# Kernel tuning notes

Measured on AMD Instinct MI355X. Metric: run time of the kernel, lower is better.

The kernel has to match this reference:

```python
import jax, jax.numpy as jnp
import numpy as np

N_NODES, SEQ_LEN, IN_CH, HID, OUT_CH, N_EDGES = 10000, 12, 16, 64, 1, 160000


def setup_inputs() -> dict:
    key = jax.random.key(0)
    ks = jax.random.split(key, 16)
    s = 1.0 / np.sqrt(HID)
    u = lambda k, shape: jax.random.uniform(k, shape, jnp.float32, -s, s)
    return {
        "x_seq": jax.random.normal(ks[0], (1, SEQ_LEN, N_NODES, IN_CH), jnp.float32),
        "edge_index": jax.random.randint(ks[1], (2, N_EDGES), 0, N_NODES, jnp.int32),
        "gcn_w": jax.random.normal(ks[2], (IN_CH, HID), jnp.float32) / np.sqrt(IN_CH),
        "gcn_b": jnp.zeros((HID,), jnp.float32),
        "w_ih0": u(ks[3], (3 * HID, HID)),
        "w_hh0": u(ks[4], (3 * HID, HID)),
        "b_ih0": u(ks[5], (3 * HID,)),
        "b_hh0": u(ks[6], (3 * HID,)),
        "w_ih1": u(ks[7], (3 * HID, HID)),
        "w_hh1": u(ks[8], (3 * HID, HID)),
        "b_ih1": u(ks[9], (3 * HID,)),
        "b_hh1": u(ks[10], (3 * HID,)),
        "attn_w": u(ks[11], (HID, 1)),
        "attn_b": u(ks[12], (1,)),
        "fc_w": u(ks[13], (HID, OUT_CH)),
        "fc_b": u(ks[14], (OUT_CH,)),
    }


def _gcn_all_t(x_ntf, edge_index, w, b):
    # x_ntf: (N, T, F). Symmetric-normalized GCNConv with self loops (PyG default),
    # applied to every timestep at once (edge structure is static).
    n = x_ntf.shape[0]
    loop = jnp.arange(n, dtype=edge_index.dtype)
    src = jnp.concatenate([edge_index[0], loop])
    dst = jnp.concatenate([edge_index[1], loop])
    deg = jax.ops.segment_sum(jnp.ones_like(src, dtype=x_ntf.dtype), dst, num_segments=n)
    dis = jax.lax.rsqrt(deg)  # deg >= 1 thanks to self loops
    norm = dis[src] * dis[dst]  # (E+N,)
    msg = x_ntf[src] * norm[:, None, None]  # (E+N, T, F)
    agg = jax.ops.segment_sum(msg, dst, num_segments=n)  # (N, T, F)
    return agg @ w + b  # (N, T, H)


def _gru_layer(x, w_ih, w_hh, b_ih, b_hh):
    # x: (B, T, Hin) batch_first; PyTorch GRU cell equations, h0 = 0.
    bsz, _, _ = x.shape
    h_dim = w_hh.shape[1]
    xi = x @ w_ih.T + b_ih  # (B, T, 3H), precomputed input projections

    def step(h, xt):
        gh = h @ w_hh.T + b_hh
        ir, iz, in_ = jnp.split(xt, 3, axis=-1)
        hr, hz, hn = jnp.split(gh, 3, axis=-1)
        r = jax.nn.sigmoid(ir + hr)
        z = jax.nn.sigmoid(iz + hz)
        n = jnp.tanh(in_ + r * hn)
        h_new = (1.0 - z) * n + z * h
        return h_new, h_new

    h0 = jnp.zeros((bsz, h_dim), x.dtype)
    _, hs = jax.lax.scan(step, h0, jnp.swapaxes(xi, 0, 1))  # (T, B, H)
    return jnp.swapaxes(hs, 0, 1)


def reference(x_seq, edge_index, gcn_w, gcn_b, w_ih0, w_hh0, b_ih0, b_hh0,
              w_ih1, w_hh1, b_ih1, b_hh1, attn_w, attn_b, fc_w, fc_b):
    batch, seq_len, num_nodes, _ = x_seq.shape  # batch == 1 (see notes)
    # (B, T, N, F) -> (N, T, F)
    x_ntf = jnp.swapaxes(x_seq[0], 0, 1)
    gcn_out = jax.nn.relu(_gcn_all_t(x_ntf, edge_index, gcn_w, gcn_b))  # (N, T, H)
    # gru_input: (B*N, T, H); dropout between GRU layers disabled (inference)
    h1 = _gru_layer(gcn_out, w_ih0, w_hh0, b_ih0, b_hh0)
    gru_out = _gru_layer(h1, w_ih1, w_hh1, b_ih1, b_hh1)  # (N, T, H)
    attn_scores = jax.nn.softmax(gru_out @ attn_w + attn_b, axis=1)  # (N, T, 1)
    context = jnp.sum(attn_scores * gru_out, axis=1)  # (N, H)
    residual = (context @ fc_w + fc_b).reshape(batch, num_nodes, -1)
    last_known = x_seq[:, -1, :, 0][..., None]  # (B, N, 1)
    return last_known + residual
```

## Files before the change

### kernel.cpp

```cpp
#include <hip/hip_runtime.h>
#include <hip/hip_bf16.h>
#include <hip/hip_fp16.h>

#define N_NODES 10000
#define SEQ_T 12
#define IN_CH 16
#define HID 64
#define N_EDGES 160000
#define CAP 96
#define PB 0xAAAAAAAAu

typedef __attribute__((ext_vector_type(8))) short short8;
typedef __attribute__((ext_vector_type(4))) float floatx4;

__device__ __forceinline__ float frcp(float x){ return __builtin_amdgcn_rcpf(x); }
__device__ __forceinline__ float sigmf(float x){ return frcp(1.0f + __expf(-x)); }
__device__ __forceinline__ float tanh_fast(float x){ return 1.0f - 2.0f * frcp(1.0f + __expf(2.0f * x)); }
__device__ __forceinline__ unsigned short f2bf(float f){
  union { float f; unsigned int u; } c; c.f = f;
  unsigned int u = c.u;
  return (unsigned short)((u + 0x7FFFu + ((u >> 16) & 1u)) >> 16);
}
__device__ __forceinline__ unsigned short f2h(float f){
  _Float16 h = (_Float16)f; unsigned short u; __builtin_memcpy(&u, &h, 2); return u;
}
__device__ __forceinline__ unsigned int cvt_pk_bf16(float a, float b){
  unsigned int r;
  asm("v_cvt_pk_bf16_f32 %0, %1, %2" : "=v"(r) : "v"(a), "v"(b));
  return r;
}


__global__ void k_fill(const int* __restrict__ ei, unsigned int* __restrict__ cnt,
                       int* __restrict__ csr,
                       const float* __restrict__ wih0, const float* __restrict__ whh0,
                       const float* __restrict__ wih1, const float* __restrict__ whh1,
                       unsigned short* __restrict__ wF,
                       const float* __restrict__ x, unsigned short* __restrict__ xT){
  int i = blockIdx.x * 256 + threadIdx.x;
  if (i < 49152){
    const float* srcs[4] = {wih0, whh0, wih1, whh1};
    int p = i / 12288, ii = i - p * 12288;
    int e = ii & 7, l = (ii >> 3) & 63, jk = ii >> 9;
    int kt = jk / 12, jt = jk - kt * 12;
    int j = (l & 15) + 16 * jt;
    int k = ((l >> 4) * 8) + e + 32 * kt;
    wF[i] = f2bf(srcs[p][j * 64 + k]);
  }
  {
    int n = i >> 4, ch = i & 15;
    const float* xp = x + (size_t)n * IN_CH + ch;
    unsigned short tmp[SEQ_T];
    #pragma unroll
    for (int t = 0; t < SEQ_T; ++t) tmp[t] = f2h(xp[(size_t)t * N_NODES * IN_CH]);
    unsigned short* dp = xT + (size_t)n * 192 + ch * 12;
    *(ushort4*)(dp)     = make_ushort4(tmp[0], tmp[1], tmp[2],  tmp[3]);
    *(ushort4*)(dp + 4) = make_ushort4(tmp[4], tmp[5], tmp[6],  tmp[7]);
    *(ushort4*)(dp + 8) = make_ushort4(tmp[8], tmp[9], tmp[10], tmp[11]);
  }
  int s = ei[i], d = ei[N_EDGES + i];
  unsigned int pos = atomicAdd(&cnt[d], 1u) - PB;
  if (pos < CAP) csr[d * CAP + pos] = s;
}

__global__ __launch_bounds__(256, 3) void k_fused(
    const float* __restrict__ x, const unsigned short* __restrict__ xT,
    const unsigned int* __restrict__ cnt, const int* __restrict__ csr,
    const float* __restrict__ gcn_w, const float* __restrict__ gcn_b,
    const unsigned short* __restrict__ wF,
    const float* __restrict__ bih0, const float* __restrict__ bhh0,
    const float* __restrict__ bih1, const float* __restrict__ bhh1,
    const float* __restrict__ attn_w, const float* __restrict__ fc_w,
    const float* __restrict__ fc_b, float* __restrict__ out){
  __shared__ union {
    struct {
      float sm[SEQ_T][16][17];
      float smw[IN_CH * HID];
      float smb[HID];
      int2  eLDS[16][16];
    } A;
    struct {
      unsigned short HL[SEQ_T][16][72];
      float scdc[SEQ_T][2][16];
    } B;
  } U;
  __shared__ union {
    unsigned short gout[SEQ_T][1024];
    unsigned short h1[2][16][72];
  } V;

  const int tid = threadIdx.x;
  const int blk = blockIdx.x;

  {
    for (int i = tid; i < IN_CH * HID; i += 256) U.A.smw[i] = gcn_w[i];
    if (tid < HID) U.A.smb[tid] = gcn_b[tid];
    const int g = tid >> 4, ch = tid & 15;
    const int dst = blk * 16 + g;
    int deg = (int)(cnt[dst] - PB);
    if (deg > CAP) deg = CAP;
    float selfdis = rsqrtf((float)deg + 1.0f);
    __half2 ah[6];
    {
      const __half2* xs = (const __half2*)(const void*)(xT + (size_t)dst * 192 + ch * 12);
      __half2 sd2 = __float2half2_rn(selfdis);
      #pragma unroll
      for (int k = 0; k < 6; ++k) ah[k] = __hmul2(sd2, xs[k]);
    }
    for (int base = 0; base < deg; base += 16){
      int ep = base + ch;
      int2 ev = make_int2(0, 0);
      if (ep < deg){
        int s = csr[dst * CAP + ep];
        ev = make_int2(s, __float_as_int(rsqrtf((float)(cnt[s] - PB) + 1.0f)));
      }
      U.A.eLDS[g][ch] = ev;
      int c2 = deg - base; if (c2 > 16) c2 = 16;
      #pragma unroll 4
      for (int j = 0; j < c2; ++j){
        int2 e2 = U.A.eLDS[g][j];
        __half2 wh = __float2half2_rn(__int_as_float(e2.y));
        const __half2* xp = (const __half2*)(const void*)(xT + (size_t)e2.x * 192 + ch * 12);
        #pragma unroll
        for (int k = 0; k < 6; ++k) ah[k] = __hfma2(wh, xp[k], ah[k]);
      }
    }
    #pragma unroll
    for (int t = 0; t < SEQ_T; ++t){
      float f = (t & 1) ? __high2float(ah[t >> 1]) : __low2float(ah[t >> 1]);
      U.A.sm[t][g][ch] = selfdis * f;
    }
    __syncthreads();
    const int hq = tid & 15;
    float wreg[16][4];
    #pragma unroll
    for (int f = 0; f < 16; ++f)
      #pragma unroll
      for (int j = 0; j < 4; ++j) wreg[f][j] = U.A.smw[f * HID + hq * 4 + j];
    float b0 = U.A.smb[hq * 4],     b1 = U.A.smb[hq * 4 + 1],
          b2 = U.A.smb[hq * 4 + 2], b3 = U.A.smb[hq * 4 + 3];
    const int lb = (hq >> 3) * 512 + (g + 16 * ((hq >> 1) & 3)) * 8 + (hq & 1) * 4;
    #pragma unroll
    for (int t = 0; t < SEQ_T; ++t){
      float o0 = b0, o1 = b1, o2 = b2, o3 = b3;
      #pragma unroll
      for (int f = 0; f < 16; ++f){
        float v = U.A.sm[t][g][f];
        o0 = fmaf(v, wreg[f][0], o0);
        o1 = fmaf(v, wreg[f][1], o1);
        o2 = fmaf(v, wreg[f][2], o2);
        o3 = fmaf(v, wreg[f][3], o3);
      }
      unsigned int plo = cvt_pk_bf16(fmaxf(o0, 0.0f), fmaxf(o1, 0.0f));
      unsigned int phi = cvt_pk_bf16(fmaxf(o2, 0.0f), fmaxf(o3, 0.0f));
      *(uint2*)(void*)(&V.gout[t][lb]) = make_uint2(plo, phi);
    }
    __syncthreads();
  }

  const int w = tid >> 6;
  const int l = tid & 63;
  const int c = l & 15;
  const int q = l >> 4;
  const int hbase = 16 * w + 4 * q;

  {
    floatx4 brz4, bzz4, bin4, bhn4;
    #pragma unroll
    for (int r = 0; r < 4; ++r){
      brz4[r] = bih0[hbase + r] + bhh0[hbase + r];
      bzz4[r] = bih0[64 + hbase + r] + bhh0[64 + hbase + r];
      bin4[r] = bih0[128 + hbase + r];
      bhn4[r] = bhh0[128 + hbase + r];
    }
    short8 bw[2][3][2];
    #pragma unroll
    for (int g2 = 0; g2 < 2; ++g2)
      #pragma unroll
      for (int s = 0; s < 3; ++s)
        #pragma unroll
        for (int kt = 0; kt < 2; ++kt){
          int jt = w + 4 * s;
          size_t idx = ((((size_t)g2 * 2 + kt) * 12 + jt) * 64 + l) * 8;
          bw[g2][s][kt] = *(const short8*)(wF + idx);
        }
    float hp[4] = {0.f, 0.f, 0.f, 0.f};
    for (int t = 0; t < SEQ_T; ++t){
      short8 xa0 = *(const short8*)&V.gout[t][l * 8];
      short8 xa1 = *(const short8*)&V.gout[t][512 + l * 8];
      floatx4 aR = brz4, aZ = bzz4, aNx = bin4, aNh = bhn4;
      if (t > 0){
        short8 ha0 = *(const short8*)&U.B.HL[t - 1][c][8 * q];
        short8 ha1 = *(const short8*)&U.B.HL[t - 1][c][8 * q + 32];
        aR  = __builtin_amdgcn_mfma_f32_16x16x32_bf16(bw[1][0][0], ha0, aR, 0, 0, 0);
        aR  = __builtin_amdgcn_mfma_f32_16x16x32_bf16(bw[1][0][1], ha1, aR, 0, 0, 0);
        aZ  = __builtin_amdgcn_mfma_f32_16x16x32_bf16(bw[1][1][0], ha0, aZ, 0, 0, 0);
        aZ  = __builtin_amdgcn_mfma_f32_16x16x32_bf16(bw[1][1][1], ha1, aZ, 0, 0, 0);
        aNh = __builtin_amdgcn_mfma_f32_16x16x32_bf16(bw[1][2][0], ha0, aNh, 0, 0, 0);
        aNh = __builtin_amdgcn_mfma_f32_16x16x32_bf16(bw[1][2][1], ha1, aNh, 0, 0, 0);
      }
      aR  = __builtin_amdgcn_mfma_f32_16x16x32_bf16(bw[0][0][0], xa0, aR, 0, 0, 0);
      aR  = __builtin_amdgcn_mfma_f32_16x16x32_bf16(bw[0][0][1], xa1, aR, 0, 0, 0);
      aZ  = __builtin_amdgcn_mfma_f32_16x16x32_bf16(bw[0][1][0], xa0, aZ, 0, 0, 0);
      aZ  = __builtin_amdgcn_mfma_f32_16x16x32_bf16(bw[0][1][1], xa1, aZ, 0, 0, 0);
      aNx = __builtin_amdgcn_mfma_f32_16x16x32_bf16(bw[0][2][0], xa0, aNx, 0, 0, 0);
      aNx = __builtin_amdgcn_mfma_f32_16x16x32_bf16(bw[0][2][1], xa1, aNx, 0, 0, 0);
      float h4[4];
      #pragma unroll
      for (int r = 0; r < 4; ++r){
        float rr = sigmf(aR[r]);
        float zz = sigmf(aZ[r]);
        float nn = tanh_fast(aNx[r] + rr * aNh[r]);
        h4[r] = nn + zz * (hp[r] - nn);
        hp[r] = h4[r];
      }
      *(uint2*)(void*)(&U.B.HL[t][c][hbase]) =
          make_uint2(cvt_pk_bf16(h4[0], h4[1]), cvt_pk_bf16(h4[2], h4[3]));
      __syncthreads();
    }
  }

  short8 bwA[2];
  #pragma unroll
  for (int kt = 0; kt < 2; ++kt){
    short8 v;
    #pragma unroll
    for (int e = 0; e < 8; ++e){
      int k = q * 8 + e + 32 * kt;
      float f = (c == 0) ? attn_w[k] : (c == 1) ? fc_w[k] : 0.0f;
      v[e] = (short)f2bf(f);
    }
    bwA[kt] = v;
  }

  {
    floatx4 brz4, bzz4, bin4, bhn4;
    #pragma unroll
    for (int r = 0; r < 4; ++r){
      brz4[r] = bih1[hbase + r] + bhh1[hbase + r];
      bzz4[r] = bih1[64 + hbase + r] + bhh1[64 + hbase + r];
      bin4[r] = bih1[128 + hbase + r];
      bhn4[r] = bhh1[128 + hbase + r];
    }
    short8 bw[2][3][2];
    #pragma unroll
    for (int g2 = 0; g2 < 2; ++g2)
      #pragma unroll
      for (int s = 0; s < 3; ++s)
        #pragma unroll
        for (int kt = 0; kt < 2; ++kt){
          int jt = w + 4 * s;
          size_t idx = ((((size_t)(2 + g2) * 2 + kt) * 12 + jt) * 64 + l) * 8;
          bw[g2][s][kt] = *(const short8*)(wF + idx);
        }
    float hp[4] = {0.f, 0.f, 0.f, 0.f};
    for (int t = 0; t < SEQ_T; ++t){
      int pr = t & 1;
      short8 xa0 = *(const short8*)&U.B.HL[t][c][8 * q];
      short8 xa1 = *(const short8*)&U.B.HL[t][c][8 * q + 32];
      floatx4 aR = brz4, aZ = bzz4, aNx = bin4, aNh = bhn4;
      if (t > 0){
        short8 ha0 = *(const short8*)&V.h1[pr][c][8 * q];
        short8 ha1 = *(const short8*)&V.h1[pr][c][8 * q + 32];
        aR  = __builtin_amdgcn_mfma_f32_16x16x32_bf16(bw[1][0][0], ha0, aR, 0, 0, 0);
        aR  = __builtin_amdgcn_mfma_f32_16x16x32_bf16(bw[1][0][1], ha1, aR, 0, 0, 0);
        aZ  = __builtin_amdgcn_mfma_f32_16x16x32_bf16(bw[1][1][0], ha0, aZ, 0, 0, 0);
        aZ  = __builtin_amdgcn_mfma_f32_16x16x32_bf16(bw[1][1][1], ha1, aZ, 0, 0, 0);
        aNh = __builtin_amdgcn_mfma_f32_16x16x32_bf16(bw[1][2][0], ha0, aNh, 0, 0, 0);
        aNh = __builtin_amdgcn_mfma_f32_16x16x32_bf16(bw[1][2][1], ha1, aNh, 0, 0, 0);
        if (w == 0){
          floatx4 aA = (floatx4){0.f, 0.f, 0.f, 0.f};
          aA = __builtin_amdgcn_mfma_f32_16x16x32_bf16(bwA[0], ha0, aA, 0, 0, 0);
          aA = __builtin_amdgcn_mfma_f32_16x16x32_bf16(bwA[1], ha1, aA, 0, 0, 0);
          if (q == 0){
            U.B.scdc[t - 1][0][c] = aA[0];
            U.B.scdc[t - 1][1][c] = aA[1];
          }
        }
      }
      aR  = __builtin_amdgcn_mfma_f32_16x16x32_bf16(bw[0][0][0], xa0, aR, 0, 0, 0);
      aR  = __builtin_amdgcn_mfma_f32_16x16x32_bf16(bw[0][0][1], xa1, aR, 0, 0, 0);
      aZ  = __builtin_amdgcn_mfma_f32_16x16x32_bf16(bw[0][1][0], xa0, aZ, 0, 0, 0);
      aZ  = __builtin_amdgcn_mfma_f32_16x16x32_bf16(bw[0][1][1], xa1, aZ, 0, 0, 0);
      aNx = __builtin_amdgcn_mfma_f32_16x16x32_bf16(bw[0][2][0], xa0, aNx, 0, 0, 0);
      aNx = __builtin_amdgcn_mfma_f32_16x16x32_bf16(bw[0][2][1], xa1, aNx, 0, 0, 0);
      float h4[4];
      #pragma unroll
      for (int r = 0; r < 4; ++r){
        float rr = sigmf(aR[r]);
        float zz = sigmf(aZ[r]);
        float nn = tanh_fast(aNx[r] + rr * aNh[r]);
        h4[r] = nn + zz * (hp[r] - nn);
        hp[r] = h4[r];
      }
      *(uint2*)(void*)(&V.h1[1 - pr][c][hbase]) =
          make_uint2(cvt_pk_bf16(h4[0], h4[1]), cvt_pk_bf16(h4[2], h4[3]));
      __syncthreads();
    }
  }

  if (w == 0){
    short8 hL0 = *(const short8*)&V.h1[0][c][8 * q];
    short8 hL1 = *(const short8*)&V.h1[0][c][8 * q + 32];
    floatx4 aA = (floatx4){0.f, 0.f, 0.f, 0.f};
    aA = __builtin_amdgcn_mfma_f32_16x16x32_bf16(bwA[0], hL0, aA, 0, 0, 0);
    aA = __builtin_amdgcn_mfma_f32_16x16x32_bf16(bwA[1], hL1, aA, 0, 0, 0);
    if (q == 0){
      U.B.scdc[SEQ_T - 1][0][c] = aA[0];
      U.B.scdc[SEQ_T - 1][1][c] = aA[1];
    }
    int gn = blk * 16 + l;
    if (l < 16){
      float sc[SEQ_T], dc[SEQ_T];
      #pragma unroll
      for (int t = 0; t < SEQ_T; ++t){ sc[t] = U.B.scdc[t][0][l]; dc[t] = U.B.scdc[t][1][l]; }
      float m = sc[0];
      #pragma unroll
      for (int t = 1; t < SEQ_T; ++t) m = fmaxf(m, sc[t]);
      float den = 0.0f, num = 0.0f;
      #pragma unroll
      for (int t = 0; t < SEQ_T; ++t){
        float p = __expf(sc[t] - m);
        den += p;
        num = fmaf(p, dc[t], num);
      }
      float y = fc_b[0] + num * frcp(den);
      float last = x[((size_t)(SEQ_T - 1) * N_NODES + gn) * IN_CH];
      out[gn] = last + y;
    }
  }
}

extern "C" void kernel_launch(void* const* d_in, const int* in_sizes, int n_in,
                              void* d_out, int out_size, void* d_ws, size_t ws_size,
                              hipStream_t stream){
  const float* x = (const float*)d_in[0];
  const int* ei  = (const int*)d_in[1];
  char* ws = (char*)d_ws;
  unsigned int*   cnt = (unsigned int*)(ws);
  int*            csr = (int*)(ws + 40960);
  unsigned short* wF  = (unsigned short*)(ws + 3880960);
  unsigned short* xT  = (unsigned short*)(ws + 3979264);

  k_fill<<<625, 256, 0, stream>>>(ei, cnt, csr,
      (const float*)d_in[4], (const float*)d_in[5],
      (const float*)d_in[8], (const float*)d_in[9], wF,
      x, xT);
  k_fused<<<625, 256, 0, stream>>>(
      x, xT, cnt, csr,
      (const float*)d_in[2], (const float*)d_in[3], wF,
      (const float*)d_in[6],  (const float*)d_in[7],
      (const float*)d_in[10], (const float*)d_in[11],
      (const float*)d_in[12], (const float*)d_in[14], (const float*)d_in[15],
      (float*)d_out);
}
```

Measured before the change: 138.0 us.

## Interleave the two GRU layers in one software-pipelined time loop

The two sequential GRU layer loops are merged into one loop of SEQ_T+1 iterations: layer 1 computes step t while layer 0 computes step t+1, with one barrier per iteration. This roughly halves the number of block-wide barriers and gives the scheduler two independent MFMA and transcendental chains to overlap, aimed at cutting latency on the serial recurrence. Layer-0 outputs now go through a 2-deep ring buffer instead of a full 12-step buffer, and gout and h1 become separate shared arrays instead of a union. Both layers' weight fragments and biases are held in registers at once, which raises VGPR pressure under the 3-blocks-per-CU launch bound and risks spills. A small change in the fill kernel swaps a local pointer array for a ternary select.

Result: slower. 147.0 us (+6.5%).

```diff
diff --git a/kernel.cpp b/kernel.cpp
--- a/kernel.cpp
+++ b/kernel.cpp
@@ -39,13 +39,13 @@
                        const float* __restrict__ x, unsigned short* __restrict__ xT){
   int i = blockIdx.x * 256 + threadIdx.x;
   if (i < 49152){
-    const float* srcs[4] = {wih0, whh0, wih1, whh1};
     int p = i / 12288, ii = i - p * 12288;
+    const float* sp = (p & 2) ? ((p & 1) ? whh1 : wih1) : ((p & 1) ? whh0 : wih0);
     int e = ii & 7, l = (ii >> 3) & 63, jk = ii >> 9;
     int kt = jk / 12, jt = jk - kt * 12;
     int j = (l & 15) + 16 * jt;
     int k = ((l >> 4) * 8) + e + 32 * kt;
-    wF[i] = f2bf(srcs[p][j * 64 + k]);
+    wF[i] = f2bf(sp[j * 64 + k]);
   }
   {
     int n = i >> 4, ch = i & 15;
@@ -80,14 +80,12 @@
       int2  eLDS[16][16];
     } A;
     struct {
-      unsigned short HL[SEQ_T][16][72];
+      unsigned short HL[2][16][72];
       float scdc[SEQ_T][2][16];
     } B;
   } U;
-  __shared__ union {
-    unsigned short gout[SEQ_T][1024];
-    unsigned short h1[2][16][72];
-  } V;
+  __shared__ unsigned short gout[SEQ_T][1024];
+  __shared__ unsigned short h1[2][16][72];
 
   const int tid = threadIdx.x;
   const int blk = blockIdx.x;
@@ -153,7 +151,7 @@
       }
       unsigned int plo = cvt_pk_bf16(fmaxf(o0, 0.0f), fmaxf(o1, 0.0f));
       unsigned int phi = cvt_pk_bf16(fmaxf(o2, 0.0f), fmaxf(o3, 0.0f));
-      *(uint2*)(void*)(&V.gout[t][lb]) = make_uint2(plo, phi);
+      *(uint2*)(void*)(&gout[t][lb]) = make_uint2(plo, phi);
     }
     __syncthreads();
   }
@@ -164,144 +162,126 @@
   const int q = l >> 4;
   const int hbase = 16 * w + 4 * q;
 
-  {
-    floatx4 brz4, bzz4, bin4, bhn4;
-    #pragma unroll
-    for (int r = 0; r < 4; ++r){
-      brz4[r] = bih0[hbase + r] + bhh0[hbase + r];
-      bzz4[r] = bih0[64 + hbase + r] + bhh0[64 + hbase + r];
-      bin4[r] = bih0[128 + hbase + r];
-      bhn4[r] = bhh0[128 + hbase + r];
-    }
-    short8 bw[2][3][2];
-    #pragma unroll
-    for (int g2 = 0; g2 < 2; ++g2)
-      #pragma unroll
-      for (int s = 0; s < 3; ++s)
-        #pragma unroll
-        for (int kt = 0; kt < 2; ++kt){
-          int jt = w + 4 * s;
-          size_t idx = ((((size_t)g2 * 2 + kt) * 12 + jt) * 64 + l) * 8;
-          bw[g2][s][kt] = *(const short8*)(wF + idx);
-        }
-    float hp[4] = {0.f, 0.f, 0.f, 0.f};
-    for (int t = 0; t < SEQ_T; ++t){
-      short8 xa0 = *(const short8*)&V.gout[t][l * 8];
-      short8 xa1 = *(const short8*)&V.gout[t][512 + l * 8];
-      floatx4 aR = brz4, aZ = bzz4, aNx = bin4, aNh = bhn4;
-      if (t > 0){
-        short8 ha0 = *(const short8*)&U.B.HL[t - 1][c][8 * q];
-        short8 ha1 = *(const short8*)&U.B.HL[t - 1][c][8 * q + 32];
-        aR  = __builtin_amdgcn_mfma_f32_16x16x32_bf16(bw[1][0][0], ha0, aR, 0, 0, 0);
-        aR  = __builtin_amdgcn_mfma_f32_16x16x32_bf16(bw[1][0][1], ha1, aR, 0, 0, 0);
-        aZ  = __builtin_amdgcn_mfma_f32_16x16x32_bf16(bw[1][1][0], ha0, aZ, 0, 0, 0);
-        aZ  = __builtin_amdgcn_mfma_f32_16x16x32_bf16(bw[1][1][1], ha1, aZ, 0, 0, 0);
-        aNh = __builtin_amdgcn_mfma_f32_16x16x32_bf16(bw[1][2][0], ha0, aNh, 0, 0, 0);
-        aNh = __builtin_amdgcn_mfma_f32_16x16x32_bf16(bw[1][2][1], ha1, aNh, 0, 0, 0);
-      }
-      aR  = __builtin_amdgcn_mfma_f32_16x16x32_bf16(bw[0][0][0], xa0, aR, 0, 0, 0);
-      aR  = __builtin_amdgcn_mfma_f32_16x16x32_bf16(bw[0][0][1], xa1, aR, 0, 0, 0);
-      aZ  = __builtin_amdgcn_mfma_f32_16x16x32_bf16(bw[0][1][0], xa0, aZ, 0, 0, 0);
-      aZ  = __builtin_amdgcn_mfma_f32_16x16x32_bf16(bw[0][1][1], xa1, aZ, 0, 0, 0);
-      aNx = __builtin_amdgcn_mfma_f32_16x16x32_bf16(bw[0][2][0], xa0, aNx, 0, 0, 0);
-      aNx = __builtin_amdgcn_mfma_f32_16x16x32_bf16(bw[0][2][1], xa1, aNx, 0, 0, 0);
+  floatx4 brz0, bzz0, bin0, bhn0, brz1, bzz1, bin1, bhn1;
+  #pragma unroll
+  for (int r = 0; r < 4; ++r){
+    brz0[r] = bih0[hbase + r] + bhh0[hbase + r];
+    bzz0[r] = bih0[64 + hbase + r] + bhh0[64 + hbase + r];
+    bin0[r] = bih0[128 + hbase + r];
+    bhn0[r] = bhh0[128 + hbase + r];
+    brz1[r] = bih1[hbase + r] + bhh1[hbase + r];
+    bzz1[r] = bih1[64 + hbase + r] + bhh1[64 + hbase + r];
+    bin1[r] = bih1[128 + hbase + r];
+    bhn1[r] = bhh1[128 + hbase + r];
+  }
+  short8 bw0[2][3][2], bw1[2][3][2];
+  #pragma unroll
+  for (int g2 = 0; g2 < 2; ++g2)
+    #pragma unroll
+    for (int s = 0; s < 3; ++s)
+      #pragma unroll
+      for (int kt = 0; kt < 2; ++kt){
+        int jt = w + 4 * s;
+        bw0[g2][s][kt] = *(const short8*)(wF + ((((size_t)g2 * 2 + kt) * 12 + jt) * 64 + l) * 8);
+        bw1[g2][s][kt] = *(const short8*)(wF + ((((size_t)(2 + g2) * 2 + kt) * 12 + jt) * 64 + l) * 8);
+      }
+  short8 bwA[2];
+  #pragma unroll
+  for (int kt = 0; kt < 2; ++kt){
+    short8 v;
+    #pragma unroll
+    for (int e = 0; e < 8; ++e){
+      int k = q * 8 + e + 32 * kt;
+      float f = (c == 0) ? attn_w[k] : (c == 1) ? fc_w[k] : 0.0f;
+      v[e] = (short)f2bf(f);
+    }
+    bwA[kt] = v;
+  }
+
+  float hp0[4] = {0.f, 0.f, 0.f, 0.f};
+  float hp1[4] = {0.f, 0.f, 0.f, 0.f};
+  for (int i = 0; i <= SEQ_T; ++i){
+    if (i < SEQ_T){
+      short8 xa0 = *(const short8*)&gout[i][l * 8];
+      short8 xa1 = *(const short8*)&gout[i][512 + l * 8];
+      floatx4 aR = brz0, aZ = bzz0, aNx = bin0, aNh = bhn0;
+      if (i > 0){
+        short8 ha0 = *(const short8*)&U.B.HL[(i - 1) & 1][c][8 * q];
+        short8 ha1 = *(const short8*)&U.B.HL[(i - 1) & 1][c][8 * q + 32];
+        aR  = __builtin_amdgcn_mfma_f32_16x16x32_bf16(bw0[1][0][0], ha0, aR, 0, 0, 0);
+        aR  = __builtin_amdgcn_mfma_f32_16x16x32_bf16(bw0[1][0][1], ha1, aR, 0, 0, 0);
+        aZ  = __builtin_amdgcn_mfma_f32_16x16x32_bf16(bw0[1][1][0], ha0, aZ, 0, 0, 0);
+        aZ  = __builtin_amdgcn_mfma_f32_16x16x32_bf16(bw0[1][1][1], ha1, aZ, 0, 0, 0);
+        aNh = __builtin_amdgcn_mfma_f32_16x16x32_bf16(bw0[1][2][0], ha0, aNh, 0, 0, 0);
+        aNh = __builtin_amdgcn_mfma_f32_16x16x32_bf16(bw0[1][2][1], ha1, aNh, 0, 0, 0);
+      }
+      aR  = __builtin_amdgcn_mfma_f32_16x16x32_bf16(bw0[0][0][0], xa0, aR, 0, 0, 0);
+      aR  = __builtin_amdgcn_mfma_f32_16x16x32_bf16(bw0[0][0][1], xa1, aR, 0, 0, 0);
+      aZ  = __builtin_amdgcn_mfma_f32_16x16x32_bf16(bw0[0][1][0], xa0, aZ, 0, 0, 0);
+      aZ  = __builtin_amdgcn_mfma_f32_16x16x32_bf16(bw0[0][1][1], xa1, aZ, 0, 0, 0);
+      aNx = __builtin_amdgcn_mfma_f32_16x16x32_bf16(bw0[0][2][0], xa0, aNx, 0, 0, 0);
+      aNx = __builtin_amdgcn_mfma_f32_16x16x32_bf16(bw0[0][2][1], xa1, aNx, 0, 0, 0);
       float h4[4];
       #pragma unroll
       for (int r = 0; r < 4; ++r){
         float rr = sigmf(aR[r]);
         float zz = sigmf(aZ[r]);
         float nn = tanh_fast(aNx[r] + rr * aNh[r]);
-        h4[r] = nn + zz * (hp[r] - nn);
-        hp[r] = h4[r];
-      }
-      *(uint2*)(void*)(&U.B.HL[t][c][hbase]) =
+        h4[r] = nn + zz * (hp0[r] - nn);
+        hp0[r] = h4[r];
+      }
+      *(uint2*)(void*)(&U.B.HL[i & 1][c][hbase]) =
           make_uint2(cvt_pk_bf16(h4[0], h4[1]), cvt_pk_bf16(h4[2], h4[3]));
-      __syncthreads();
-    }
-  }
-
-  short8 bwA[2];
-  #pragma unroll
-  for (int kt = 0; kt < 2; ++kt){
-    short8 v;
-    #pragma unroll
-    for (int e = 0; e < 8; ++e){
-      int k = q * 8 + e + 32 * kt;
-      float f = (c == 0) ? attn_w[k] : (c == 1) ? fc_w[k] : 0.0f;
-      v[e] = (short)f2bf(f);
-    }
-    bwA[kt] = v;
-  }
-
-  {
-    floatx4 brz4, bzz4, bin4, bhn4;
-    #pragma unroll
-    for (int r = 0; r < 4; ++r){
-      brz4[r] = bih1[hbase + r] + bhh1[hbase + r];
-      bzz4[r] = bih1[64 + hbase + r] + bhh1[64 + hbase + r];
-      bin4[r] = bih1[128 + hbase + r];
-      bhn4[r] = bhh1[128 + hbase + r];
-    }
-    short8 bw[2][3][2];
-    #pragma unroll
-    for (int g2 = 0; g2 < 2; ++g2)
-      #pragma unroll
-      for (int s = 0; s < 3; ++s)
-        #pragma unroll
-        for (int kt = 0; kt < 2; ++kt){
-          int jt = w + 4 * s;
-          size_t idx = ((((size_t)(2 + g2) * 2 + kt) * 12 + jt) * 64 + l) * 8;
-          bw[g2][s][kt] = *(const short8*)(wF + idx);
-        }
-    float hp[4] = {0.f, 0.f, 0.f, 0.f};
-    for (int t = 0; t < SEQ_T; ++t){
+    }
+    if (i >= 1){
+      int t = i - 1;
       int pr = t & 1;
-      short8 xa0 = *(const short8*)&U.B.HL[t][c][8 * q];
-      short8 xa1 = *(const short8*)&U.B.HL[t][c][8 * q + 32];
-      floatx4 aR = brz4, aZ = bzz4, aNx = bin4, aNh = bhn4;
+      short8 xb0 = *(const short8*)&U.B.HL[pr][c][8 * q];
+      short8 xb1 = *(const short8*)&U.B.HL[pr][c][8 * q + 32];
+      floatx4 aR = brz1, aZ = bzz1, aNx = bin1, aNh = bhn1;
       if (t > 0){
-        short8 ha0 = *(const short8*)&V.h1[pr][c][8 * q];
-        short8 ha1 = *(const short8*)&V.h1[pr][c][8 * q + 32];
-        aR  = __builtin_amdgcn_mfma_f32_16x16x32_bf16(bw[1][0][0], ha0, aR, 0, 0, 0);
-        aR  = __builtin_amdgcn_mfma_f32_16x16x32_bf16(bw[1][0][1], ha1, aR, 0, 0, 0);
-        aZ  = __builtin_amdgcn_mfma_f32_16x16x32_bf16(bw[1][1][0], ha0, aZ, 0, 0, 0);
-        aZ  = __builtin_amdgcn_mfma_f32_16x16x32_bf16(bw[1][1][1], ha1, aZ, 0, 0, 0);
-        aNh = __builtin_amdgcn_mfma_f32_16x16x32_bf16(bw[1][2][0], ha0, aNh, 0, 0, 0);
-        aNh = __builtin_amdgcn_mfma_f32_16x16x32_bf16(bw[1][2][1], ha1, aNh, 0, 0, 0);
+        short8 hb0 = *(const short8*)&h1[pr][c][8 * q];
+        short8 hb1 = *(const short8*)&h1[pr][c][8 * q + 32];
+        aR  = __builtin_amdgcn_mfma_f32_16x16x32_bf16(bw1[1][0][0], hb0, aR, 0, 0, 0);
+        aR  = __builtin_amdgcn_mfma_f32_16x16x32_bf16(bw1[1][0][1], hb1, aR, 0, 0, 0);
+        aZ  = __builtin_amdgcn_mfma_f32_16x16x32_bf16(bw1[1][1][0], hb0, aZ, 0, 0, 0);
+        aZ  = __builtin_amdgcn_mfma_f32_16x16x32_bf16(bw1[1][1][1], hb1, aZ, 0, 0, 0);
+        aNh = __builtin_amdgcn_mfma_f32_16x16x32_bf16(bw1[1][2][0], hb0, aNh, 0, 0, 0);
+        aNh = __builtin_amdgcn_mfma_f32_16x16x32_bf16(bw1[1][2][1], hb1, aNh, 0, 0, 0);
         if (w == 0){
           floatx4 aA = (floatx4){0.f, 0.f, 0.f, 0.f};
-          aA = __builtin_amdgcn_mfma_f32_16x16x32_bf16(bwA[0], ha0, aA, 0, 0, 0);
-          aA = __builtin_amdgcn_mfma_f32_16x16x32_bf16(bwA[1], ha1, aA, 0, 0, 0);
+          aA = __builtin_amdgcn_mfma_f32_16x16x32_bf16(bwA[0], hb0, aA, 0, 0, 0);
+          aA = __builtin_amdgcn_mfma_f32_16x16x32_bf16(bwA[1], hb1, aA, 0, 0, 0);
           if (q == 0){
             U.B.scdc[t - 1][0][c] = aA[0];
             U.B.scdc[t - 1][1][c] = aA[1];
           }
         }
       }
-      aR  = __builtin_amdgcn_mfma_f32_16x16x32_bf16(bw[0][0][0], xa0, aR, 0, 0, 0);
-      aR  = __builtin_amdgcn_mfma_f32_16x16x32_bf16(bw[0][0][1], xa1, aR, 0, 0, 0);
-      aZ  = __builtin_amdgcn_mfma_f32_16x16x32_bf16(bw[0][1][0], xa0, aZ, 0, 0, 0);
-      aZ  = __builtin_amdgcn_mfma_f32_16x16x32_bf16(bw[0][1][1], xa1, aZ, 0, 0, 0);
-      aNx = __builtin_amdgcn_mfma_f32_16x16x32_bf16(bw[0][2][0], xa0, aNx, 0, 0, 0);
-      aNx = __builtin_amdgcn_mfma_f32_16x16x32_bf16(bw[0][2][1], xa1, aNx, 0, 0, 0);
+      aR  = __builtin_amdgcn_mfma_f32_16x16x32_bf16(bw1[0][0][0], xb0, aR, 0, 0, 0);
+      aR  = __builtin_amdgcn_mfma_f32_16x16x32_bf16(bw1[0][0][1], xb1, aR, 0, 0, 0);
+      aZ  = __builtin_amdgcn_mfma_f32_16x16x32_bf16(bw1[0][1][0], xb0, aZ, 0, 0, 0);
+      aZ  = __builtin_amdgcn_mfma_f32_16x16x32_bf16(bw1[0][1][1], xb1, aZ, 0, 0, 0);
+      aNx = __builtin_amdgcn_mfma_f32_16x16x32_bf16(bw1[0][2][0], xb0, aNx, 0, 0, 0);
+      aNx = __builtin_amdgcn_mfma_f32_16x16x32_bf16(bw1[0][2][1], xb1, aNx, 0, 0, 0);
       float h4[4];
       #pragma unroll
       for (int r = 0; r < 4; ++r){
         float rr = sigmf(aR[r]);
         float zz = sigmf(aZ[r]);
         float nn = tanh_fast(aNx[r] + rr * aNh[r]);
-        h4[r] = nn + zz * (hp[r] - nn);
-        hp[r] = h4[r];
-      }
-      *(uint2*)(void*)(&V.h1[1 - pr][c][hbase]) =
+        h4[r] = nn + zz * (hp1[r] - nn);
+        hp1[r] = h4[r];
+      }
+      *(uint2*)(void*)(&h1[1 - pr][c][hbase]) =
           make_uint2(cvt_pk_bf16(h4[0], h4[1]), cvt_pk_bf16(h4[2], h4[3]));
-      __syncthreads();
-    }
+    }
+    __syncthreads();
   }
 
   if (w == 0){
-    short8 hL0 = *(const short8*)&V.h1[0][c][8 * q];
-    short8 hL1 = *(const short8*)&V.h1[0][c][8 * q + 32];
+    short8 hL0 = *(const short8*)&h1[0][c][8 * q];
+    short8 hL1 = *(const short8*)&h1[0][c][8 * q + 32];
     floatx4 aA = (floatx4){0.f, 0.f, 0.f, 0.f};
     aA = __builtin_amdgcn_mfma_f32_16x16x32_bf16(bwA[0], hL0, aA, 0, 0, 0);
     aA = __builtin_amdgcn_mfma_f32_16x16x32_bf16(bwA[1], hL1, aA, 0, 0, 0);
```
